# Kernel tuning notes

Measured on AMD Instinct MI355X. Metric: run time of the kernel, lower is better.

Reference implementation:

```python
import jax, jax.numpy as jnp
import numpy as np

B, T, N, M = 512, 128, 256, 128

def setup_inputs() -> dict:
    key = jax.random.key(0)
    ks = jax.random.split(key, 7)
    s = 0.05
    return {
        "X": jax.random.normal(ks[0], (B, T, N), jnp.float32),
        "W_e": jax.random.normal(ks[1], (T, 2 * M + T), jnp.float32) * s,   # WU_e.weight
        "v_e": jax.random.normal(ks[2], (1, T), jnp.float32) * s,           # v_e.weight
        "W_ih": jax.random.normal(ks[3], (4 * M, N), jnp.float32) * s,
        "W_hh": jax.random.normal(ks[4], (4 * M, M), jnp.float32) * s,
        "b_ih": jax.random.normal(ks[5], (4 * M,), jnp.float32) * s,
        "b_hh": jax.random.normal(ks[6], (4 * M,), jnp.float32) * s,
    }

def reference(X, W_e, v_e, W_ih, W_hh, b_ih, b_hh):
    b, t_len, n = X.shape
    m = W_hh.shape[1]
    # Split WU_e into the part applied to [h;c] (cols :2m) and to X rows (cols 2m:)
    W_hs, W_x = W_e[:, : 2 * m], W_e[:, 2 * m :]           # [T,2m], [T,T]
    Xp = jnp.swapaxes(X, 1, 2)                              # [B,n,T] driving series per feature
    feat_proj = jnp.einsum('bnt,st->bns', Xp, W_x)          # time-invariant part of attention
    v = v_e[0]                                              # [T]

    def step(carry, x_t):
        h, c = carry                                        # [B,m] each
        hs = jnp.concatenate([h, c], axis=-1)               # [B,2m]
        tanh_act = jnp.tanh((hs @ W_hs.T)[:, None, :] + feat_proj)  # [B,n,T]
        E = jnp.einsum('bns,s->bn', tanh_act, v)             # [B,n]
        alpha = jax.nn.softmax(E, axis=1)
        x_tilde = x_t * alpha                                # [B,n]
        gates = x_tilde @ W_ih.T + b_ih + h @ W_hh.T + b_hh  # [B,4m]
        i, f, g, o = jnp.split(gates, 4, axis=-1)            # torch gate order i,f,g,o
        i = jax.nn.sigmoid(i); f = jax.nn.sigmoid(f)
        g = jnp.tanh(g);       o = jax.nn.sigmoid(o)
        c2 = f * c + i * g
        h2 = o * jnp.tanh(c2)
        return (h2, c2), h2

    h0 = jnp.zeros((b, m), X.dtype)
    c0 = jnp.zeros((b, m), X.dtype)
    _, Hs = jax.lax.scan(step, (h0, c0), jnp.swapaxes(X, 0, 1))  # xs: [T,B,n]
    return Hs  # [T,B,m]
```

## Files before the change

### kernel.cpp

```cpp
#include <hip/hip_runtime.h>
#include <hip/hip_bf16.h>

#define Bb 512
#define Tt 128
#define Nn 256
#define Mm 128

typedef __bf16 bf16_t;
typedef __bf16 bf16x8 __attribute__((ext_vector_type(8)));
typedef float f32x4 __attribute__((ext_vector_type(4)));
typedef unsigned u32x4 __attribute__((ext_vector_type(4)));

__device__ __forceinline__ float bflo(unsigned u) { return __uint_as_float(u << 16); }
__device__ __forceinline__ float bfhi(unsigned u) { return __uint_as_float(u & 0xffff0000u); }

__device__ __forceinline__ float fast_sigmoid(float x) {
  return __builtin_amdgcn_rcpf(1.f + __expf(-x));
}
__device__ __forceinline__ float fast_tanh(float x) {
  float e = __expf(2.f * x);
  return 1.f - 2.f * __builtin_amdgcn_rcpf(e + 1.f);
}

__global__ void prep_whs(const float* __restrict__ W_e, bf16_t* __restrict__ Whs_pk) {
  int blk = blockIdx.x;
  int st = blk >> 3, kk = blk & 7;
  int lane = threadIdx.x;
  int s = st * 16 + (lane & 15);
  int m0 = kk * 32 + (lane >> 4) * 8;
  bf16_t v[8];
#pragma unroll
  for (int j = 0; j < 8; ++j) v[j] = (bf16_t)W_e[s * 384 + m0 + j];
  *(bf16x8*)(Whs_pk + ((size_t)blk * 64 + lane) * 8) = *(bf16x8*)v;
}

__global__ void prep_wp(const float* __restrict__ W_ih, const float* __restrict__ W_hh,
                        const float* __restrict__ b_ih, const float* __restrict__ b_hh,
                        bf16_t* __restrict__ Wp_pk, float* __restrict__ bp) {
  int blk = blockIdx.x;
  int gt = blk / 12, kk = blk % 12;
  int lane = threadIdx.x;
  int r = gt * 16 + (lane & 15);
  int mt = r >> 6, type = (r >> 4) & 3, ml = r & 15;
  int g = type * 128 + mt * 16 + ml;
  int k0 = kk * 32 + (lane >> 4) * 8;
  bf16_t v[8];
#pragma unroll
  for (int j = 0; j < 8; ++j) {
    int k = k0 + j;
    float wv = (k < 256) ? W_ih[g * 256 + k] : W_hh[g * 128 + (k - 256)];
    v[j] = (bf16_t)wv;
  }
  *(bf16x8*)(Wp_pk + ((size_t)blk * 64 + lane) * 8) = *(bf16x8*)v;
  if (kk == 0 && lane < 16) bp[r] = b_ih[g] + b_hh[g];
}

__global__ __launch_bounds__(256) void featproj_kernel(
    const float* __restrict__ X, const float* __restrict__ W_e, bf16_t* __restrict__ F) {
  int b  = blockIdx.x >> 2;
  int s0 = (blockIdx.x & 3) << 5;
  int tid = threadIdx.x;
  __shared__ float Xs[32][256];
  float acc[32];
#pragma unroll
  for (int i = 0; i < 32; ++i) acc[i] = 0.f;
  for (int tc = 0; tc < 4; ++tc) {
    __syncthreads();
#pragma unroll
    for (int i = 0; i < 32; ++i)
      Xs[i][tid] = X[((size_t)b * Tt + tc * 32 + i) * Nn + tid];
    __syncthreads();
    for (int tt = 0; tt < 32; ++tt) {
      float xv = Xs[tt][tid];
#pragma unroll
      for (int ss = 0; ss < 32; ++ss)
        acc[ss] = fmaf(W_e[(s0 + ss) * 384 + 256 + tc * 32 + tt], xv, acc[ss]);
    }
  }
#pragma unroll
  for (int ss = 0; ss < 32; ++ss)
    F[((size_t)b * 128 + s0 + ss) * 256 + tid] = (bf16_t)__expf(2.f * acc[ss]);
}

#define BCAST(x) __builtin_bit_cast(bf16x8, x)

__global__ __launch_bounds__(512, 2) void fused_kernel(
    const float* __restrict__ X, const bf16_t* __restrict__ F,
    const bf16_t* __restrict__ Whs_pk, const bf16_t* __restrict__ Wp_pk,
    const float* __restrict__ bp, const float* __restrict__ v_e,
    float* __restrict__ out) {
  __shared__ __align__(16) bf16_t Fl[2][128][256];
  __shared__ __align__(16) bf16_t Abuf[16][520];
  __shared__ float2 avL[2][128];
  __shared__ float  Ep[8][256];

  int bid = blockIdx.x;
  int b0 = 2 * ((bid & 7) * 32 + (bid >> 3));
  int tid = threadIdx.x;
  int w = tid >> 6, lane = tid & 63;
  int fr = lane & 15, ksel = lane >> 4;

  u32x4 wq[48];
  u32x4 hq[8];
  {
    const u32x4* wp4 = (const u32x4*)Wp_pk;
#pragma unroll
    for (int j = 0; j < 4; ++j)
#pragma unroll
      for (int kk = 0; kk < 12; ++kk)
        wq[j * 12 + kk] = wp4[(size_t)((4 * w + j) * 12 + kk) * 64 + lane];
    const u32x4* wh4 = (const u32x4*)Whs_pk;
#pragma unroll
    for (int kk = 0; kk < 8; ++kk)
      hq[kk] = wh4[(size_t)(w * 8 + kk) * 64 + lane];
#pragma unroll
    for (int i = 0; i < 48; ++i) asm volatile("" : "+v"(wq[i]));
#pragma unroll
    for (int i = 0; i < 8; ++i) asm volatile("" : "+v"(hq[i]));
  }
  float biasr[4];
#pragma unroll
  for (int j = 0; j < 4; ++j) biasr[j] = bp[(4 * w + j) * 16 + fr];
  float vmr = -2.f * v_e[w * 16 + fr];
  float c0r = 0.f, c1r = 0.f;

  {
    const u32x4* src = (const u32x4*)(F + (size_t)b0 * 32768);
    u32x4* dst = (u32x4*)&Fl[0][0][0];
    for (int i = tid; i < 8192; i += 512) dst[i] = src[i];
    u32x4 z = {0, 0, 0, 0};
    u32x4* ab = (u32x4*)&Abuf[0][0];
    for (int i = tid; i < 1040; i += 512) ab[i] = z;
  }
  __syncthreads();

  for (int t = 0; t < Tt; ++t) {
    float4 xpre = make_float4(0.f, 0.f, 0.f, 0.f);
    if (w < 2)
      xpre = *(const float4*)(X + ((size_t)(b0 + w) * Tt + t) * Nn + 4 * lane);

    {
      f32x4 pa = {0.f, 0.f, 0.f, 0.f};
#pragma unroll
      for (int kk = 0; kk < 8; ++kk) {
        bf16x8 af = *(const bf16x8*)&Abuf[fr][256 + kk * 32 + ksel * 8];
        pa = __builtin_amdgcn_mfma_f32_16x16x32_bf16(af, BCAST(hq[kk]), pa, 0, 0, 0);
      }
      if (ksel == 0) {
        int s = w * 16 + fr;
        avL[0][s] = make_float2(__expf(2.f * pa[0]), vmr);
        avL[1][s] = make_float2(__expf(2.f * pa[1]), vmr);
      }
    }
    __syncthreads();

    {
      int ab = w >> 2, sq = (w & 3) * 32;
      const bf16_t* frow = &Fl[ab][sq][4 * lane];
      f32x4 En = {0.f, 0.f, 0.f, 0.f};
#pragma unroll 8
      for (int s = 0; s < 32; ++s) {
        float2 avv = avL[ab][sq + s];
        uint2 u = *(const uint2*)(frow + s * 256);
        En[0] = fmaf(avv.y, __builtin_amdgcn_rcpf(fmaf(avv.x, bflo(u.x), 1.f)), En[0]);
        En[1] = fmaf(avv.y, __builtin_amdgcn_rcpf(fmaf(avv.x, bfhi(u.x), 1.f)), En[1]);
        En[2] = fmaf(avv.y, __builtin_amdgcn_rcpf(fmaf(avv.x, bflo(u.y), 1.f)), En[2]);
        En[3] = fmaf(avv.y, __builtin_amdgcn_rcpf(fmaf(avv.x, bfhi(u.y), 1.f)), En[3]);
      }
      *(f32x4*)&Ep[w][4 * lane] = En;
    }
    __syncthreads();

    if (w < 2) {
      int n0 = 4 * lane;
      f32x4 E  = *(const f32x4*)&Ep[w * 4 + 0][n0];
      f32x4 e1 = *(const f32x4*)&Ep[w * 4 + 1][n0];
      f32x4 e2 = *(const f32x4*)&Ep[w * 4 + 2][n0];
      f32x4 e3 = *(const f32x4*)&Ep[w * 4 + 3][n0];
      E = E + e1 + e2 + e3;
      float p0 = __expf(E[0]), p1 = __expf(E[1]), p2 = __expf(E[2]), p3 = __expf(E[3]);
      float tot = (p0 + p1) + (p2 + p3);
#pragma unroll
      for (int off = 32; off; off >>= 1) tot += __shfl_xor(tot, off, 64);
      float ir = __builtin_amdgcn_rcpf(tot);
      bf16_t xb[4];
      xb[0] = (bf16_t)(xpre.x * (p0 * ir));
      xb[1] = (bf16_t)(xpre.y * (p1 * ir));
      xb[2] = (bf16_t)(xpre.z * (p2 * ir));
      xb[3] = (bf16_t)(xpre.w * (p3 * ir));
      *(uint2*)&Abuf[w][n0] = *(uint2*)xb;
    }
    __syncthreads();

    float h0w = 0.f, c0w = 0.f, h1w = 0.f, c1w = 0.f;
    {
      f32x4 acg0 = {0,0,0,0}, acg1 = {0,0,0,0}, acg2 = {0,0,0,0}, acg3 = {0,0,0,0};
#pragma unroll
      for (int kk = 0; kk < 12; ++kk) {
        bf16x8 af = *(const bf16x8*)&Abuf[fr][kk * 32 + ksel * 8];
        acg0 = __builtin_amdgcn_mfma_f32_16x16x32_bf16(af, BCAST(wq[0 * 12 + kk]), acg0, 0, 0, 0);
        acg1 = __builtin_amdgcn_mfma_f32_16x16x32_bf16(af, BCAST(wq[1 * 12 + kk]), acg1, 0, 0, 0);
        acg2 = __builtin_amdgcn_mfma_f32_16x16x32_bf16(af, BCAST(wq[2 * 12 + kk]), acg2, 0, 0, 0);
        acg3 = __builtin_amdgcn_mfma_f32_16x16x32_bf16(af, BCAST(wq[3 * 12 + kk]), acg3, 0, 0, 0);
      }
      if (ksel == 0) {
        int m = w * 16 + fr;
        {
          float ig = fast_sigmoid(acg0[0] + biasr[0]);
          float fg = fast_sigmoid(acg1[0] + biasr[1]);
          float gg = fast_tanh   (acg2[0] + biasr[2]);
          float og = fast_sigmoid(acg3[0] + biasr[3]);
          c0w = fg * c0r + ig * gg;  h0w = og * fast_tanh(c0w);  c0r = c0w;
        }
        {
          float ig = fast_sigmoid(acg0[1] + biasr[0]);
          float fg = fast_sigmoid(acg1[1] + biasr[1]);
          float gg = fast_tanh   (acg2[1] + biasr[2]);
          float og = fast_sigmoid(acg3[1] + biasr[3]);
          c1w = fg * c1r + ig * gg;  h1w = og * fast_tanh(c1w);  c1r = c1w;
        }
        out[((size_t)t * Bb + b0) * Mm + m]     = h0w;
        out[((size_t)t * Bb + b0 + 1) * Mm + m] = h1w;
      }
    }
    __syncthreads();
    if (ksel == 0) {
      int m = w * 16 + fr;
      Abuf[0][256 + m] = (bf16_t)h0w;
      Abuf[0][384 + m] = (bf16_t)c0w;
      Abuf[1][256 + m] = (bf16_t)h1w;
      Abuf[1][384 + m] = (bf16_t)c1w;
    }
    __syncthreads();
  }
}

extern "C" void kernel_launch(void* const* d_in, const int* in_sizes, int n_in,
                              void* d_out, int out_size, void* d_ws, size_t ws_size,
                              hipStream_t stream) {
  const float* X    = (const float*)d_in[0];
  const float* W_e  = (const float*)d_in[1];
  const float* v_e  = (const float*)d_in[2];
  const float* W_ih = (const float*)d_in[3];
  const float* W_hh = (const float*)d_in[4];
  const float* b_ih = (const float*)d_in[5];
  const float* b_hh = (const float*)d_in[6];
  float* out = (float*)d_out;

  char* ws = (char*)d_ws;
  bf16_t* F      = (bf16_t*)ws;
  bf16_t* Whs_pk = (bf16_t*)(ws + 33554432);
  bf16_t* Wp_pk  = (bf16_t*)(ws + 33619968);
  float*  bp     = (float*) (ws + 34013184);

  prep_whs<<<64, 64, 0, stream>>>(W_e, Whs_pk);
  prep_wp<<<384, 64, 0, stream>>>(W_ih, W_hh, b_ih, b_hh, Wp_pk, bp);
  featproj_kernel<<<2048, 256, 0, stream>>>(X, W_e, F);
  fused_kernel<<<256, 512, 0, stream>>>(X, F, Whs_pk, Wp_pk, bp, v_e, out);
}
```

Before: 912.4 us.

## Software-pipeline the two batch rows so attention overlaps the LSTM gate MFMAs

```diff
diff --git a/kernel.cpp b/kernel.cpp
--- a/kernel.cpp
+++ b/kernel.cpp
@@ -83,6 +83,7 @@
 }
 
 #define BCAST(x) __builtin_bit_cast(bf16x8, x)
+#define MFMA16(a, b, c) __builtin_amdgcn_mfma_f32_16x16x32_bf16((a), (b), (c), 0, 0, 0)
 
 __global__ __launch_bounds__(512, 2) void fused_kernel(
     const float* __restrict__ X, const bf16_t* __restrict__ F,
@@ -94,11 +95,11 @@
   __shared__ float2 avL[2][128];
   __shared__ float  Ep[8][256];
 
-  int bid = blockIdx.x;
-  int b0 = 2 * ((bid & 7) * 32 + (bid >> 3));
-  int tid = threadIdx.x;
-  int w = tid >> 6, lane = tid & 63;
-  int fr = lane & 15, ksel = lane >> 4;
+  const int bid = blockIdx.x;
+  const int base = 2 * ((bid & 7) * 32 + (bid >> 3));
+  const int tid = threadIdx.x;
+  const int w = tid >> 6, lane = tid & 63;
+  const int fr = lane & 15, ksel = lane >> 4;
 
   u32x4 wq[48];
   u32x4 hq[8];
@@ -121,118 +122,115 @@
   float biasr[4];
 #pragma unroll
   for (int j = 0; j < 4; ++j) biasr[j] = bp[(4 * w + j) * 16 + fr];
-  float vmr = -2.f * v_e[w * 16 + fr];
+  const float vmr = -2.f * v_e[w * 16 + fr];
   float c0r = 0.f, c1r = 0.f;
 
   {
-    const u32x4* src = (const u32x4*)(F + (size_t)b0 * 32768);
+    const u32x4* src = (const u32x4*)(F + (size_t)base * 32768);
     u32x4* dst = (u32x4*)&Fl[0][0][0];
     for (int i = tid; i < 8192; i += 512) dst[i] = src[i];
     u32x4 z = {0, 0, 0, 0};
     u32x4* ab = (u32x4*)&Abuf[0][0];
     for (int i = tid; i < 1040; i += 512) ab[i] = z;
   }
+  if (ksel == 0) avL[0][w * 16 + fr] = make_float2(1.f, vmr);
   __syncthreads();
 
-  for (int t = 0; t < Tt; ++t) {
-    float4 xpre = make_float4(0.f, 0.f, 0.f, 0.f);
-    if (w < 2)
-      xpre = *(const float4*)(X + ((size_t)(b0 + w) * Tt + t) * Nn + 4 * lane);
-
-    {
-      f32x4 pa = {0.f, 0.f, 0.f, 0.f};
-#pragma unroll
-      for (int kk = 0; kk < 8; ++kk) {
-        bf16x8 af = *(const bf16x8*)&Abuf[fr][256 + kk * 32 + ksel * 8];
-        pa = __builtin_amdgcn_mfma_f32_16x16x32_bf16(af, BCAST(hq[kk]), pa, 0, 0, 0);
-      }
-      if (ksel == 0) {
-        int s = w * 16 + fr;
-        avL[0][s] = make_float2(__expf(2.f * pa[0]), vmr);
-        avL[1][s] = make_float2(__expf(2.f * pa[1]), vmr);
-      }
-    }
-    __syncthreads();
-
-    {
-      int ab = w >> 2, sq = (w & 3) * 32;
-      const bf16_t* frow = &Fl[ab][sq][4 * lane];
-      f32x4 En = {0.f, 0.f, 0.f, 0.f};
-#pragma unroll 8
-      for (int s = 0; s < 32; ++s) {
-        float2 avv = avL[ab][sq + s];
-        uint2 u = *(const uint2*)(frow + s * 256);
+  auto ph1 = [&](int b, int tau) {
+    f32x4 pa = {0.f, 0.f, 0.f, 0.f};
+#pragma unroll
+    for (int kk = 0; kk < 8; ++kk) {
+      bf16x8 af = *(const bf16x8*)&Abuf[fr][256 + kk * 32 + ksel * 8];
+      pa = MFMA16(af, BCAST(hq[kk]), pa);
+    }
+    if (ksel == 0) {
+      float a = (tau & 1) ? (b ? pa[3] : pa[2]) : (b ? pa[1] : pa[0]);
+      avL[b][w * 16 + fr] = make_float2(__expf(2.f * a), vmr);
+    }
+  };
+
+  auto ph3 = [&](int b, int tau, float4 xp) {
+    int n0 = 4 * lane;
+    f32x4 E = *(const f32x4*)&Ep[0][n0];
+#pragma unroll
+    for (int r = 1; r < 8; ++r) E = E + *(const f32x4*)&Ep[r][n0];
+    float p0 = __expf(E[0]), p1 = __expf(E[1]), p2 = __expf(E[2]), p3 = __expf(E[3]);
+    float tot = (p0 + p1) + (p2 + p3);
+#pragma unroll
+    for (int off = 32; off; off >>= 1) tot += __shfl_xor(tot, off, 64);
+    float ir = __builtin_amdgcn_rcpf(tot);
+    bf16_t xb[4];
+    xb[0] = (bf16_t)(xp.x * (p0 * ir));
+    xb[1] = (bf16_t)(xp.y * (p1 * ir));
+    xb[2] = (bf16_t)(xp.z * (p2 * ir));
+    xb[3] = (bf16_t)(xp.w * (p3 * ir));
+    *(uint2*)&Abuf[b + 2 * (tau & 1)][n0] = *(uint2*)xb;
+  };
+
+  auto region13 = [&](int ab, int gb, int tau, float& cr, bool do4, bool do2) {
+    f32x4 acg0 = {0,0,0,0}, acg1 = {0,0,0,0}, acg2 = {0,0,0,0}, acg3 = {0,0,0,0};
+    f32x4 En = {0.f, 0.f, 0.f, 0.f};
+    const bf16_t* frow = &Fl[ab][w * 16][0] + 4 * lane;
+#pragma unroll
+    for (int i = 0; i < 16; ++i) {
+      if (do2) {
+        float2 avv = avL[ab][w * 16 + i];
+        uint2 u = *(const uint2*)(frow + i * 256);
         En[0] = fmaf(avv.y, __builtin_amdgcn_rcpf(fmaf(avv.x, bflo(u.x), 1.f)), En[0]);
         En[1] = fmaf(avv.y, __builtin_amdgcn_rcpf(fmaf(avv.x, bfhi(u.x), 1.f)), En[1]);
         En[2] = fmaf(avv.y, __builtin_amdgcn_rcpf(fmaf(avv.x, bflo(u.y), 1.f)), En[2]);
         En[3] = fmaf(avv.y, __builtin_amdgcn_rcpf(fmaf(avv.x, bfhi(u.y), 1.f)), En[3]);
       }
-      *(f32x4*)&Ep[w][4 * lane] = En;
-    }
-    __syncthreads();
-
-    if (w < 2) {
-      int n0 = 4 * lane;
-      f32x4 E  = *(const f32x4*)&Ep[w * 4 + 0][n0];
-      f32x4 e1 = *(const f32x4*)&Ep[w * 4 + 1][n0];
-      f32x4 e2 = *(const f32x4*)&Ep[w * 4 + 2][n0];
-      f32x4 e3 = *(const f32x4*)&Ep[w * 4 + 3][n0];
-      E = E + e1 + e2 + e3;
-      float p0 = __expf(E[0]), p1 = __expf(E[1]), p2 = __expf(E[2]), p3 = __expf(E[3]);
-      float tot = (p0 + p1) + (p2 + p3);
-#pragma unroll
-      for (int off = 32; off; off >>= 1) tot += __shfl_xor(tot, off, 64);
-      float ir = __builtin_amdgcn_rcpf(tot);
-      bf16_t xb[4];
-      xb[0] = (bf16_t)(xpre.x * (p0 * ir));
-      xb[1] = (bf16_t)(xpre.y * (p1 * ir));
-      xb[2] = (bf16_t)(xpre.z * (p2 * ir));
-      xb[3] = (bf16_t)(xpre.w * (p3 * ir));
-      *(uint2*)&Abuf[w][n0] = *(uint2*)xb;
-    }
-    __syncthreads();
-
-    float h0w = 0.f, c0w = 0.f, h1w = 0.f, c1w = 0.f;
-    {
-      f32x4 acg0 = {0,0,0,0}, acg1 = {0,0,0,0}, acg2 = {0,0,0,0}, acg3 = {0,0,0,0};
-#pragma unroll
-      for (int kk = 0; kk < 12; ++kk) {
-        bf16x8 af = *(const bf16x8*)&Abuf[fr][kk * 32 + ksel * 8];
-        acg0 = __builtin_amdgcn_mfma_f32_16x16x32_bf16(af, BCAST(wq[0 * 12 + kk]), acg0, 0, 0, 0);
-        acg1 = __builtin_amdgcn_mfma_f32_16x16x32_bf16(af, BCAST(wq[1 * 12 + kk]), acg1, 0, 0, 0);
-        acg2 = __builtin_amdgcn_mfma_f32_16x16x32_bf16(af, BCAST(wq[2 * 12 + kk]), acg2, 0, 0, 0);
-        acg3 = __builtin_amdgcn_mfma_f32_16x16x32_bf16(af, BCAST(wq[3 * 12 + kk]), acg3, 0, 0, 0);
+      if (do4 && i < 12) {
+        bf16x8 af = *(const bf16x8*)&Abuf[fr][i * 32 + ksel * 8];
+        acg0 = MFMA16(af, BCAST(wq[i]),      acg0);
+        acg1 = MFMA16(af, BCAST(wq[12 + i]), acg1);
+        acg2 = MFMA16(af, BCAST(wq[24 + i]), acg2);
+        acg3 = MFMA16(af, BCAST(wq[36 + i]), acg3);
       }
+    }
+    if (do2) *(f32x4*)&Ep[w][4 * lane] = En;
+    if (do4) {
+      int par = tau & 1;
+      float g0 = par ? (gb ? acg0[3] : acg0[2]) : (gb ? acg0[1] : acg0[0]);
+      float g1 = par ? (gb ? acg1[3] : acg1[2]) : (gb ? acg1[1] : acg1[0]);
+      float g2 = par ? (gb ? acg2[3] : acg2[2]) : (gb ? acg2[1] : acg2[0]);
+      float g3 = par ? (gb ? acg3[3] : acg3[2]) : (gb ? acg3[1] : acg3[0]);
+      float ig = fast_sigmoid(g0 + biasr[0]);
+      float fg = fast_sigmoid(g1 + biasr[1]);
+      float gg = fast_tanh   (g2 + biasr[2]);
+      float og = fast_sigmoid(g3 + biasr[3]);
+      float cw = fg * cr + ig * gg;
+      float hw = og * fast_tanh(cw);
+      cr = cw;
       if (ksel == 0) {
         int m = w * 16 + fr;
-        {
-          float ig = fast_sigmoid(acg0[0] + biasr[0]);
-          float fg = fast_sigmoid(acg1[0] + biasr[1]);
-          float gg = fast_tanh   (acg2[0] + biasr[2]);
-          float og = fast_sigmoid(acg3[0] + biasr[3]);
-          c0w = fg * c0r + ig * gg;  h0w = og * fast_tanh(c0w);  c0r = c0w;
-        }
-        {
-          float ig = fast_sigmoid(acg0[1] + biasr[0]);
-          float fg = fast_sigmoid(acg1[1] + biasr[1]);
-          float gg = fast_tanh   (acg2[1] + biasr[2]);
-          float og = fast_sigmoid(acg3[1] + biasr[3]);
-          c1w = fg * c1r + ig * gg;  h1w = og * fast_tanh(c1w);  c1r = c1w;
-        }
-        out[((size_t)t * Bb + b0) * Mm + m]     = h0w;
-        out[((size_t)t * Bb + b0 + 1) * Mm + m] = h1w;
+        int wr = gb + 2 * ((tau + 1) & 1);
+        Abuf[wr][256 + m] = (bf16_t)hw;
+        Abuf[wr][384 + m] = (bf16_t)cw;
+        out[((size_t)tau * Bb + base + gb) * Mm + m] = hw;
       }
     }
-    __syncthreads();
-    if (ksel == 0) {
-      int m = w * 16 + fr;
-      Abuf[0][256 + m] = (bf16_t)h0w;
-      Abuf[0][384 + m] = (bf16_t)c0w;
-      Abuf[1][256 + m] = (bf16_t)h1w;
-      Abuf[1][384 + m] = (bf16_t)c1w;
-    }
-    __syncthreads();
-  }
+  };
+
+  for (int t = 0; t < Tt; ++t) {
+    float4 x0 = make_float4(0.f, 0.f, 0.f, 0.f), x1 = x0;
+    if (w == 0) {
+      x0 = *(const float4*)(X + ((size_t)(base)     * Tt + t) * Nn + 4 * lane);
+      x1 = *(const float4*)(X + ((size_t)(base + 1) * Tt + t) * Nn + 4 * lane);
+    }
+    region13(0, 1, t - 1, c1r, t > 0, true);
+    __syncthreads();
+    ph1(1, t);
+    if (w == 0) ph3(0, t, x0);
+    __syncthreads();
+    region13(1, 0, t, c0r, true, true);
+    __syncthreads();
+    ph1(0, t + 1);
+    if (w == 0) ph3(1, t, x1);
+    __syncthreads();
+  }
+  region13(0, 1, Tt - 1, c1r, true, false);
 }
 
 extern "C" void kernel_launch(void* const* d_in, const int* in_sizes, int n_in,
```

Result: slower. 1.933 ms (+111.8%).
